# Kernel tuning notes

Hardware: AMD Instinct MI355X
Metric: run time of the kernel (lower is better)

## Reference

```python
import jax, jax.numpy as jnp
import numpy as np

K_LAYERS = 2   # top-k layers kept in zeta routing
K_EXPERTS = 2  # top-k experts kept in alpha routing


def _topk_sparse_softmax(logits, k):
    """Keep top-k along last axis, set rest to -inf, softmax. logits [..., N]."""
    lead = logits.shape[:-1]
    n = logits.shape[-1]
    flat = logits.reshape(-1, n)
    vals, idx = jax.lax.top_k(flat, k)                      # [R,k]
    sparse = jnp.full_like(flat, -jnp.inf)
    rows = jnp.arange(flat.shape[0])[:, None]
    sparse = sparse.at[rows, idx].set(vals)
    return jax.nn.softmax(sparse, axis=-1).reshape(*lead, n)


def _lora_layer(h, W, b, A, B, zeta_l, alpha_l):
    """One backbone Linear + gated LoRA expert mixture + ReLU.
    h [B,in], W [out,in], A [E,r,in], B [E,out,r], zeta_l [B], alpha_l [B,E].
    """
    lin = h @ W.T + b                                       # [B,out]
    t = jnp.einsum('bi,eri->ber', h, A)                     # [B,E,r]
    tw = t * alpha_l[:, :, None]                            # weight experts early
    lora_sum = jnp.einsum('ber,eor->bo', tw, B)             # [B,out]
    return jax.nn.relu(lin + zeta_l[:, None] * lora_sum)


def _routing(domain_ids, dom_emb, layer_pos, Wi1, bi1, Wi2, bi2,
             Wa1, ba1, Wa2, ba2, gate_logits, R_benefit):
    M, H = dom_emb.shape
    L = layer_pos.shape[0]
    router_inp = jnp.concatenate([
        jnp.broadcast_to(dom_emb[:, None, :], (M, L, H)),
        jnp.broadcast_to(layer_pos[None, :, :], (M, L, H)),
    ], axis=-1)                                             # [M,L,2H]
    hz = jax.nn.relu(router_inp @ Wi1.T + bi1)
    zeta_logits = (hz @ Wi2.T + bi2)[..., 0]                # [M,L]
    zeta_all = _topk_sparse_softmax(zeta_logits, K_LAYERS)
    ha = jax.nn.relu(router_inp @ Wa1.T + ba1)
    alpha_logits = ha @ Wa2.T + ba2                         # [M,L,E]
    alpha_all = _topk_sparse_softmax(alpha_logits, K_EXPERTS)
    # gated benefit matrix, row-normalized
    R = jax.nn.softplus(gate_logits) * R_benefit
    R = R / jnp.clip(R.sum(-1, keepdims=True), 1e-12)
    zeta_agg = R @ zeta_all                                 # [M,L]
    alpha_agg = jnp.einsum('mn,nle->mle', R, alpha_all)     # [M,L,E]
    return zeta_agg[domain_ids], alpha_agg[domain_ids]      # [B,L],[B,L,E]


def setup_inputs() -> dict:
    key = jax.random.key(0)
    ks = jax.random.split(key, 32)
    Bsz, D0, D1, D2, D3 = 16384, 2048, 2048, 1024, 512
    E, r, M, H, L = 4, 8, 8, 64, 3
    s = 0.02
    return {
        'x': jax.random.normal(ks[0], (Bsz, D0), jnp.float32),
        'domain_ids': jax.random.randint(ks[1], (Bsz,), 0, M),
        'W1': jax.random.normal(ks[2], (D1, D0)) * s, 'b1': jnp.zeros((D1,)),
        'W2': jax.random.normal(ks[3], (D2, D1)) * s, 'b2': jnp.zeros((D2,)),
        'W3': jax.random.normal(ks[4], (D3, D2)) * s, 'b3': jnp.zeros((D3,)),
        'A1': jax.random.normal(ks[5], (E, r, D0)) * s, 'B1': jax.random.normal(ks[6], (E, D1, r)) * s,
        'A2': jax.random.normal(ks[7], (E, r, D1)) * s, 'B2': jax.random.normal(ks[8], (E, D2, r)) * s,
        'A3': jax.random.normal(ks[9], (E, r, D2)) * s, 'B3': jax.random.normal(ks[10], (E, D3, r)) * s,
        'dom_emb': jax.random.normal(ks[11], (M, H)) * s,
        'layer_pos': jax.random.normal(ks[12], (L, H)) * s,
        'Wi1': jax.random.normal(ks[13], (H, 2 * H)) * 0.1, 'bi1': jnp.zeros((H,)),
        'Wi2': jax.random.normal(ks[14], (1, H)) * 0.1, 'bi2': jnp.zeros((1,)),
        'Wa1': jax.random.normal(ks[15], (H, 2 * H)) * 0.1, 'ba1': jnp.zeros((H,)),
        'Wa2': jax.random.normal(ks[16], (E, H)) * 0.1, 'ba2': jnp.zeros((E,)),
        'gate_logits': jax.random.normal(ks[17], (M, M)) * 0.1,
        'R_benefit': jax.random.uniform(ks[18], (M, M)),
    }


def reference(x, domain_ids, W1, b1, W2, b2, W3, b3,
              A1, B1, A2, B2, A3, B3,
              dom_emb, layer_pos, Wi1, bi1, Wi2, bi2,
              Wa1, ba1, Wa2, ba2, gate_logits, R_benefit):
    zeta, alpha = _routing(domain_ids, dom_emb, layer_pos, Wi1, bi1, Wi2, bi2,
                           Wa1, ba1, Wa2, ba2, gate_logits, R_benefit)
    h = _lora_layer(x, W1, b1, A1, B1, zeta[:, 0], alpha[:, 0])
    h = _lora_layer(h, W2, b2, A2, B2, zeta[:, 1], alpha[:, 1])
    h = _lora_layer(h, W3, b3, A3, B3, zeta[:, 2], alpha[:, 2])
    return h
```

## Files before the change

### kernel.cpp

```cpp
#include <hip/hip_runtime.h>

typedef __bf16 bf16_t;
typedef __bf16 bf16x8 __attribute__((ext_vector_type(8)));
typedef __bf16 bf16x4_v __attribute__((ext_vector_type(4)));
typedef float f32x4 __attribute__((ext_vector_type(4)));

#define AS1 __attribute__((address_space(1)))
#define AS3 __attribute__((address_space(3)))

__device__ __forceinline__ void gload_lds16(const void* g, void* l) {
    __builtin_amdgcn_global_load_lds((AS1 void*)(void*)g, (AS3 void*)l, 16, 0, 0);
}

__global__ void __launch_bounds__(256) prep_kernel(
    const float* __restrict__ dom_emb, const float* __restrict__ layer_pos,
    const float* __restrict__ Wi1, const float* __restrict__ bi1,
    const float* __restrict__ Wi2, const float* __restrict__ bi2,
    const float* __restrict__ Wa1, const float* __restrict__ ba1,
    const float* __restrict__ Wa2, const float* __restrict__ ba2,
    const float* __restrict__ gate_logits, const float* __restrict__ R_benefit,
    float* __restrict__ salpha,
    const float* __restrict__ s0, const float* __restrict__ s1,
    const float* __restrict__ s2, const float* __restrict__ s3,
    const float* __restrict__ s4, const float* __restrict__ s5,
    bf16_t* __restrict__ wdst,
    const float* __restrict__ B1, const float* __restrict__ B2,
    const float* __restrict__ B3, bf16_t* __restrict__ bedst)
{
    const int blk = blockIdx.x;
    const int t = threadIdx.x;
    if (blk == 0) {
        constexpr int M = 8, L = 3, E = 4, H = 64;
        __shared__ float zl[M * L];
        __shared__ float al[M * L][E];
        __shared__ float zeta_all[M][L];
        __shared__ float alpha_all[M][L][E];
        const int ml = t >> 3, js = t & 7;
        if (ml < M * L) {
            const int m = ml / L, l = ml % L;
            float zacc = 0.f;
            float aacc[E] = {0.f, 0.f, 0.f, 0.f};
            for (int jj = 0; jj < 8; ++jj) {
                const int j = js * 8 + jj;
                float hz = bi1[j], ha = ba1[j];
                for (int i = 0; i < H; ++i) {
                    const float de = dom_emb[m * H + i];
                    const float lp = layer_pos[l * H + i];
                    hz += de * Wi1[j * 2 * H + i] + lp * Wi1[j * 2 * H + H + i];
                    ha += de * Wa1[j * 2 * H + i] + lp * Wa1[j * 2 * H + H + i];
                }
                hz = fmaxf(hz, 0.f); ha = fmaxf(ha, 0.f);
                zacc += hz * Wi2[j];
                for (int e = 0; e < E; ++e) aacc[e] += ha * Wa2[e * H + j];
            }
            #pragma unroll
            for (int off = 4; off >= 1; off >>= 1) {
                zacc += __shfl_down(zacc, off, 8);
                for (int e = 0; e < E; ++e) aacc[e] += __shfl_down(aacc[e], off, 8);
            }
            if (js == 0) {
                zl[ml] = zacc + bi2[0];
                for (int e = 0; e < E; ++e) al[ml][e] = aacc[e] + ba2[e];
            }
        }
        __syncthreads();
        if (t < M) {
            const int m = t;
            float v[3] = { zl[m * L + 0], zl[m * L + 1], zl[m * L + 2] };
            int di = 0; float dv = v[0];
            for (int i = 1; i < 3; ++i) if (v[i] <= dv) { dv = v[i]; di = i; }
            float mx = -1e30f;
            for (int i = 0; i < 3; ++i) if (i != di) mx = fmaxf(mx, v[i]);
            float s = 0.f, ev[3];
            for (int i = 0; i < 3; ++i) { ev[i] = (i == di) ? 0.f : expf(v[i] - mx); s += ev[i]; }
            for (int i = 0; i < 3; ++i) zeta_all[m][i] = ev[i] / s;
            for (int l = 0; l < L; ++l) {
                float a[4];
                for (int e = 0; e < 4; ++e) a[e] = al[m * L + l][e];
                int i1 = 0;
                for (int e = 1; e < 4; ++e) if (a[e] > a[i1]) i1 = e;
                int i2 = -1;
                for (int e = 0; e < 4; ++e) { if (e == i1) continue; if (i2 < 0 || a[e] > a[i2]) i2 = e; }
                const float mx2 = fmaxf(a[i1], a[i2]);
                const float e1 = expf(a[i1] - mx2), e2 = expf(a[i2] - mx2);
                const float ss = e1 + e2;
                for (int e = 0; e < 4; ++e) alpha_all[m][l][e] = 0.f;
                alpha_all[m][l][i1] = e1 / ss;
                alpha_all[m][l][i2] = e2 / ss;
            }
        }
        __syncthreads();
        if (t < M) {
            const int m = t;
            float Rrow[8]; float rs = 0.f;
            for (int n = 0; n < M; ++n) {
                const float g = gate_logits[m * M + n];
                const float rr = log1pf(expf(g)) * R_benefit[m * M + n];
                Rrow[n] = rr; rs += rr;
            }
            rs = fmaxf(rs, 1e-12f);
            for (int l = 0; l < L; ++l) {
                float zag = 0.f, aag[4] = {0.f, 0.f, 0.f, 0.f};
                for (int n = 0; n < M; ++n) {
                    const float w = Rrow[n] / rs;
                    zag += w * zeta_all[n][l];
                    for (int e = 0; e < 4; ++e) aag[e] += w * alpha_all[n][l][e];
                }
                for (int e = 0; e < 4; ++e) salpha[(m * L + l) * 4 + e] = zag * aag[e];
            }
        }
    } else if (blk <= 6816) {
        const int i = (blk - 1) * 256 + t;
        constexpr int b0 = 1048576;
        constexpr int b1 = b0 + 524288;
        constexpr int b2 = b1 + 131072;
        constexpr int b3 = b2 + 16384;
        constexpr int b4 = b3 + 16384;
        const float* src; int rel;
        if (i < b0)      { src = s0; rel = i; }
        else if (i < b1) { src = s1; rel = i - b0; }
        else if (i < b2) { src = s2; rel = i - b1; }
        else if (i < b3) { src = s3; rel = i - b2; }
        else if (i < b4) { src = s4; rel = i - b3; }
        else             { src = s5; rel = i - b4; }
        const float4 v = ((const float4*)src)[rel];
        bf16x4_v o;
        o[0] = (__bf16)v.x; o[1] = (__bf16)v.y; o[2] = (__bf16)v.z; o[3] = (__bf16)v.w;
        ((bf16x4_v*)wdst)[i] = o;
    } else {
        const int idx = (blk - 6817) * 256 + t;
        constexpr int c1 = 2048 * 32, c2 = c1 + 1024 * 32;
        const float* B; int rel, Dout;
        if (idx < c1)      { B = B1; rel = idx;      Dout = 2048; }
        else if (idx < c2) { B = B2; rel = idx - c1; Dout = 1024; }
        else               { B = B3; rel = idx - c2; Dout = 512; }
        const int o = rel >> 5, c = rel & 31, e = c >> 3, r = c & 7;
        bedst[idx] = (__bf16)B[((size_t)e * Dout + o) * 8 + r];
    }
}

template<bool F32IN>
__global__ void __launch_bounds__(256) tw_kernel(
    const void* __restrict__ hin, bf16_t* __restrict__ xb_out,
    const bf16_t* __restrict__ Acat, const float* __restrict__ salpha,
    const int* __restrict__ dom, const int layer, const int K,
    bf16_t* __restrict__ TWb)
{
    const int t = threadIdx.x, wid = t >> 6, lane = t & 63;
    const int rb = blockIdx.x * 64 + wid * 16;
    const int ln15 = lane & 15, kg = (lane >> 4) * 8;
    const int row = rb + ln15;
    const int Kh = K >> 1;
    f32x4 a0l = {0.f,0.f,0.f,0.f}, a1l = {0.f,0.f,0.f,0.f};
    f32x4 a0h = {0.f,0.f,0.f,0.f}, a1h = {0.f,0.f,0.f,0.f};
    const bf16_t* pa0 = Acat + (size_t)ln15 * K + kg;
    const bf16_t* pa1 = pa0 + (size_t)16 * K;
    for (int k0 = 0; k0 < Kh; k0 += 32) {
        bf16x8 al, ah;
        if constexpr (F32IN) {
            const float* px = (const float*)hin + (size_t)row * K + k0 + kg;
            const float4 x0 = *(const float4*)px;
            const float4 x1 = *(const float4*)(px + 4);
            const float4 y0 = *(const float4*)(px + Kh);
            const float4 y1 = *(const float4*)(px + Kh + 4);
            al[0] = (__bf16)x0.x; al[1] = (__bf16)x0.y; al[2] = (__bf16)x0.z; al[3] = (__bf16)x0.w;
            al[4] = (__bf16)x1.x; al[5] = (__bf16)x1.y; al[6] = (__bf16)x1.z; al[7] = (__bf16)x1.w;
            ah[0] = (__bf16)y0.x; ah[1] = (__bf16)y0.y; ah[2] = (__bf16)y0.z; ah[3] = (__bf16)y0.w;
            ah[4] = (__bf16)y1.x; ah[5] = (__bf16)y1.y; ah[6] = (__bf16)y1.z; ah[7] = (__bf16)y1.w;
            *(bf16x8*)(xb_out + (size_t)row * K + k0 + kg) = al;
            *(bf16x8*)(xb_out + (size_t)row * K + Kh + k0 + kg) = ah;
        } else {
            al = *(const bf16x8*)((const bf16_t*)hin + (size_t)row * K + k0 + kg);
            ah = *(const bf16x8*)((const bf16_t*)hin + (size_t)row * K + Kh + k0 + kg);
        }
        const bf16x8 b0l = *(const bf16x8*)(pa0 + k0);
        const bf16x8 b1l = *(const bf16x8*)(pa1 + k0);
        const bf16x8 b0h = *(const bf16x8*)(pa0 + Kh + k0);
        const bf16x8 b1h = *(const bf16x8*)(pa1 + Kh + k0);
        a0l = __builtin_amdgcn_mfma_f32_16x16x32_bf16(al, b0l, a0l, 0, 0, 0);
        a1l = __builtin_amdgcn_mfma_f32_16x16x32_bf16(al, b1l, a1l, 0, 0, 0);
        a0h = __builtin_amdgcn_mfma_f32_16x16x32_bf16(ah, b0h, a0h, 0, 0, 0);
        a1h = __builtin_amdgcn_mfma_f32_16x16x32_bf16(ah, b1h, a1h, 0, 0, 0);
    }
    const f32x4 acc0 = a0l + a0h;
    const f32x4 acc1 = a1l + a1h;
    const int rbase = rb + (lane >> 4) * 4;
    #pragma unroll
    for (int i = 0; i < 4; ++i) {
        const int r2 = rbase + i;
        const int d = dom[r2];
        const float* sa = salpha + (d * 3 + layer) * 4;
        const float s0 = sa[ln15 >> 3];
        const float s1 = sa[2 + (ln15 >> 3)];
        TWb[(size_t)r2 * 32 + ln15]      = (__bf16)(acc0[i] * s0);
        TWb[(size_t)r2 * 32 + 16 + ln15] = (__bf16)(acc1[i] * s1);
    }
}


__device__ __forceinline__ void stage_chunk32(const bf16_t* g, char* chunk, int t) {
    const int row = t >> 2;
    const int sl = t & 3;
    const int src = sl ^ (((row >> 3) & 1) << 1);
    gload_lds16(g + (size_t)row * 32 + src * 8, chunk + t * 16);
}

template<int K>
__global__ void __launch_bounds__(512, 2) gemm_lora8(
    const bf16_t* __restrict__ Abuf, const bf16_t* __restrict__ Wbuf,
    const float* __restrict__ bias, const bf16_t* __restrict__ TWb,
    const bf16_t* __restrict__ Bepi, bf16_t* __restrict__ outp,
    const int N, const int nwg_n)
{
    __shared__ __align__(1024) char lds[131072];
    const int t = threadIdx.x;
    const int wid = t >> 6, lane = t & 63;
    const int wm = wid >> 2, wn = wid & 3, wnh = wn >> 1;
    const int cpx = gridDim.x >> 3;
    const int wg = (blockIdx.x & 7) * cpx + (blockIdx.x >> 3);
    const int row0 = (wg / nwg_n) * 256, col0 = (wg % nwg_n) * 256;

    const int r15 = lane & 15;
    const int swb = ((lane >> 4) ^ (((lane >> 3) & 1) << 1)) << 4;

    const char* aBase = lds + (wm << 14) + (r15 << 6) + swb;
    const char* bBase = lds + 65536 + (wnh << 14) + ((wn & 1) << 12) + (r15 << 6) + swb;
    char* const dBase = lds + t * 16;

    const int srow = t >> 2, ssl = t & 3;
    const int ssrc = ssl ^ (((srow >> 3) & 1) << 1);
    const bf16_t* sA = Abuf + (size_t)(row0 + srow) * K + ssrc * 8;
    const bf16_t* sB = Wbuf + (size_t)(col0 + srow) * K + ssrc * 8;
    constexpr size_t halfA = (size_t)128 * K;

    f32x4 acc[8][4] = {};
    bf16x8 aF[4], bF[4];

    #define RD_A(P, KQ, MB) do { _Pragma("unroll") for (int i_ = 0; i_ < 4; ++i_) \
        aF[i_] = *(const bf16x8*)(aBase + (P)*32768 + (KQ)*8192 + ((MB)+i_)*1024); } while (0)
    #define RD_B(P, KQ) do { _Pragma("unroll") for (int n_ = 0; n_ < 4; ++n_) \
        bF[n_] = *(const bf16x8*)(bBase + (P)*32768 + (KQ)*8192 + n_*1024); } while (0)

    auto mfma16 = [&](int mbase) {
        __builtin_amdgcn_s_setprio(1);
        #pragma unroll
        for (int mf = 0; mf < 4; ++mf)
            #pragma unroll
            for (int nf = 0; nf < 4; ++nf)
                acc[mbase + mf][nf] =
                    __builtin_amdgcn_mfma_f32_16x16x32_bf16(aF[mf], bF[nf], acc[mbase + mf][nf], 0, 0, 0);
        __builtin_amdgcn_s_setprio(0);
    };
    #define BAR() __builtin_amdgcn_s_barrier()

    constexpr int NT = K >> 6;

    gload_lds16(sA,              dBase + 0);
    gload_lds16(sA + halfA,      dBase + 16384);
    gload_lds16(sB,              dBase + 65536);
    gload_lds16(sB + halfA,      dBase + 65536 + 16384);
    gload_lds16(sA + 32,         dBase + 8192);
    gload_lds16(sA + halfA + 32, dBase + 24576);
    gload_lds16(sB + 32,         dBase + 65536 + 8192);
    gload_lds16(sB + halfA + 32, dBase + 65536 + 24576);
    asm volatile("s_waitcnt vmcnt(4)" ::: "memory");
    __builtin_amdgcn_s_barrier();

    const bf16_t* pA0 = sA + 64;
    const bf16_t* pA1 = sA + halfA + 64;
    const bf16_t* pB0 = sB + 64;
    const bf16_t* pB1 = sB + halfA + 64;

    #define TILE(P, MORE, TOFF) do {                                            \
        RD_A(P, 0, 0);                                                           \
        RD_B(P, 0);                                                              \
        if (MORE) { gload_lds16(pA0 + (TOFF), dBase + ((P)^1)*32768 + 0);        \
                    gload_lds16(pA1 + (TOFF), dBase + ((P)^1)*32768 + 16384); }  \
        BAR();                                                                   \
        mfma16(0);                                                               \
        RD_A(P, 0, 4);                                                           \
        if (MORE) {                                                              \
            gload_lds16(pB0 + (TOFF), dBase + 65536 + ((P)^1)*32768 + 0);        \
            gload_lds16(pB1 + (TOFF), dBase + 65536 + ((P)^1)*32768 + 16384);    \
            asm volatile("s_waitcnt vmcnt(4)" ::: "memory");                     \
        } else {                                                                 \
            asm volatile("s_waitcnt vmcnt(0)" ::: "memory");                     \
        }                                                                        \
        BAR();                                                                   \
        mfma16(4);                                                               \
        RD_A(P, 1, 4);                                                           \
        RD_B(P, 1);                                                              \
        if (MORE) { gload_lds16(pA0 + (TOFF) + 32, dBase + ((P)^1)*32768 + 8192);  \
                    gload_lds16(pA1 + (TOFF) + 32, dBase + ((P)^1)*32768 + 24576);} \
        BAR();                                                                   \
        mfma16(4);                                                               \
        RD_A(P, 1, 0);                                                           \
        if (MORE) {                                                              \
            gload_lds16(pB0 + (TOFF) + 32, dBase + 65536 + ((P)^1)*32768 + 8192);  \
            gload_lds16(pB1 + (TOFF) + 32, dBase + 65536 + ((P)^1)*32768 + 24576); \
            asm volatile("s_waitcnt vmcnt(4)" ::: "memory");                     \
        }                                                                        \
        BAR();                                                                   \
        mfma16(0);                                                               \
    } while (0)

    #pragma unroll 1
    for (int T = 0; T < NT - 2; T += 2) {
        TILE(0, true, 0);
        TILE(1, true, 64);
        pA0 += 128; pA1 += 128; pB0 += 128; pB1 += 128;
    }
    TILE(0, true, 0);
    TILE(1, false, 64);

    {
        __builtin_amdgcn_s_barrier();
        stage_chunk32(TWb + (size_t)row0 * 32,          lds + 0,             t);
        stage_chunk32(TWb + (size_t)(row0 + 128) * 32,  lds + 16384,         t);
        stage_chunk32(Bepi + (size_t)col0 * 32,         lds + 65536,         t);
        stage_chunk32(Bepi + (size_t)(col0 + 128) * 32, lds + 65536 + 16384, t);
        asm volatile("s_waitcnt vmcnt(0)" ::: "memory");
        __builtin_amdgcn_s_barrier();
        RD_B(0, 0);
        RD_A(0, 0, 0);
        mfma16(0);
        RD_A(0, 0, 4);
        mfma16(4);
    }

    __builtin_amdgcn_s_barrier();
    {
        char* eb = lds + wid * 2048;
        const int rloc = (lane >> 4) * 4;
        const int g = lane >> 4;
        const int orow0 = row0 + wm * 128;
        const int ocol0 = col0 + wn * 64;
        float bcol[4];
        #pragma unroll
        for (int nf = 0; nf < 4; ++nf) bcol[nf] = bias[ocol0 + nf * 16 + r15];
        const int rdrow = lane >> 3;
        const int rdcolb = (lane & 7) * 16;
        const int rdoff0 = rdrow * 128 + (rdcolb ^ ((rdrow >> 2) << 5));
        const int rdoff1 = (rdrow + 8) * 128 + (rdcolb ^ (((rdrow + 8) >> 2) << 5));
        bf16_t* outbase = outp + (size_t)ocol0 + (lane & 7) * 8;
        #pragma unroll
        for (int mf = 0; mf < 8; ++mf) {
            #pragma unroll
            for (int i = 0; i < 4; ++i) {
                const int r = rloc + i;
                #pragma unroll
                for (int nf = 0; nf < 4; ++nf) {
                    const float v = fmaxf(acc[mf][nf][i] + bcol[nf], 0.f);
                    *(bf16_t*)(eb + r * 128 + ((nf ^ g) * 32 + r15 * 2)) = (__bf16)v;
                }
            }
            __builtin_amdgcn_sched_barrier(0);
            asm volatile("" ::: "memory");
            const bf16x8 v0 = *(const bf16x8*)(eb + rdoff0);
            const bf16x8 v1 = *(const bf16x8*)(eb + rdoff1);
            asm volatile("" ::: "memory");
            __builtin_amdgcn_sched_barrier(0);
            *(bf16x8*)(outbase + (size_t)(orow0 + mf * 16 + rdrow) * N) = v0;
            *(bf16x8*)(outbase + (size_t)(orow0 + mf * 16 + 8 + rdrow) * N) = v1;
        }
    }
    #undef TILE
    #undef RD_A
    #undef RD_B
    #undef BAR
}

#define BM 128
#define BN 128
#define BK 32

template<bool OUT_F32, int K>
__global__ void __launch_bounds__(256) gemm_lora(
    const bf16_t* __restrict__ Abuf, const bf16_t* __restrict__ Wbuf,
    const float* __restrict__ bias, const bf16_t* __restrict__ TWb,
    const bf16_t* __restrict__ Bepi, void* __restrict__ outp,
    const int N)
{
    __shared__ bf16_t lA[BM * BK];
    __shared__ bf16_t lB[BN * BK];
    const int t = threadIdx.x;
    const int row0 = blockIdx.y * BM;
    const int col0 = blockIdx.x * BN;
    const int wid = t >> 6, lane = t & 63;
    const int wr = wid >> 1, wc = wid & 1;
    const int ln15 = lane & 15, kg = (lane >> 4) * 8;
    const int srow = t >> 2, sg8 = (t & 3) * 8;
    const bf16_t* gA = Abuf + (size_t)(row0 + srow) * K + sg8;
    const bf16_t* gB = Wbuf + (size_t)(col0 + srow) * K + sg8;
    bf16_t* ldA  = &lA[t * 8];
    bf16_t* ldA2 = &lA[2048 + t * 8];
    bf16_t* ldB  = &lB[t * 8];
    bf16_t* ldB2 = &lB[2048 + t * 8];
    f32x4 acc[4][4] = {};
    const int aoff = (wr * 64 + ln15) * BK + kg;
    const int boff = (wc * 64 + ln15) * BK + kg;

    auto compute_tile = [&]() {
        bf16x8 af[4], bfr[4];
        #pragma unroll
        for (int m = 0; m < 4; ++m) af[m] = *(const bf16x8*)&lA[aoff + m * 16 * BK];
        #pragma unroll
        for (int n = 0; n < 4; ++n) bfr[n] = *(const bf16x8*)&lB[boff + n * 16 * BK];
        #pragma unroll
        for (int m = 0; m < 4; ++m)
            #pragma unroll
            for (int n = 0; n < 4; ++n)
                acc[m][n] = __builtin_amdgcn_mfma_f32_16x16x32_bf16(af[m], bfr[n], acc[m][n], 0, 0, 0);
    };

    constexpr size_t half = (size_t)64 * K;
    constexpr int nk = K / BK;
    #pragma unroll 1
    for (int kt = 0; kt < nk; ++kt) {
        gload_lds16(gA + kt * BK, ldA);
        gload_lds16(gA + half + kt * BK, ldA2);
        gload_lds16(gB + kt * BK, ldB);
        gload_lds16(gB + half + kt * BK, ldB2);
        __syncthreads();
        compute_tile();
        __syncthreads();
    }
    gload_lds16(TWb + (size_t)(row0 + srow) * 32 + sg8, ldA);
    gload_lds16(TWb + (size_t)(row0 + 64 + srow) * 32 + sg8, ldA2);
    gload_lds16(Bepi + (size_t)(col0 + srow) * 32 + sg8, ldB);
    gload_lds16(Bepi + (size_t)(col0 + 64 + srow) * 32 + sg8, ldB2);
    __syncthreads();
    compute_tile();

    const int orow = row0 + wr * 64 + (lane >> 4) * 4;
    const int ocol = col0 + wc * 64 + ln15;
    #pragma unroll
    for (int n = 0; n < 4; ++n) {
        const int col = ocol + n * 16;
        const float bn = bias[col];
        #pragma unroll
        for (int m = 0; m < 4; ++m) {
            const int rbase = orow + m * 16;
            #pragma unroll
            for (int i = 0; i < 4; ++i) {
                const float v = fmaxf(acc[m][n][i] + bn, 0.f);
                if constexpr (OUT_F32)
                    ((float*)outp)[(size_t)(rbase + i) * N + col] = v;
                else
                    ((bf16_t*)outp)[(size_t)(rbase + i) * N + col] = (__bf16)v;
            }
        }
    }
}

extern "C" void kernel_launch(void* const* d_in, const int* in_sizes, int n_in,
                              void* d_out, int out_size, void* d_ws, size_t ws_size,
                              hipStream_t stream)
{
    const float* x    = (const float*)d_in[0];
    const int*   dom  = (const int*)d_in[1];
    const float* W1   = (const float*)d_in[2];  const float* b1  = (const float*)d_in[3];
    const float* W2   = (const float*)d_in[4];  const float* b2  = (const float*)d_in[5];
    const float* W3   = (const float*)d_in[6];  const float* b3  = (const float*)d_in[7];
    const float* A1   = (const float*)d_in[8];  const float* B1  = (const float*)d_in[9];
    const float* A2   = (const float*)d_in[10]; const float* B2  = (const float*)d_in[11];
    const float* A3   = (const float*)d_in[12]; const float* B3  = (const float*)d_in[13];
    const float* dome = (const float*)d_in[14]; const float* lpos = (const float*)d_in[15];
    const float* Wi1  = (const float*)d_in[16]; const float* bi1 = (const float*)d_in[17];
    const float* Wi2  = (const float*)d_in[18]; const float* bi2 = (const float*)d_in[19];
    const float* Wa1  = (const float*)d_in[20]; const float* ba1 = (const float*)d_in[21];
    const float* Wa2  = (const float*)d_in[22]; const float* ba2 = (const float*)d_in[23];
    const float* gate = (const float*)d_in[24]; const float* Rb  = (const float*)d_in[25];
    (void)in_sizes; (void)n_in; (void)out_size; (void)ws_size;

    constexpr int Bsz = 16384, D0 = 2048, D1 = 2048, D2 = 1024, D3 = 512;

    char* ws = (char*)d_ws;
    size_t off = 0;
    auto alloc = [&](size_t bytes) -> void* {
        void* p = ws + off;
        off = (off + bytes + 255) & ~(size_t)255;
        return p;
    };
    float*  salpha = (float*) alloc(8 * 3 * 4 * sizeof(float));
    bf16_t* W1b = (bf16_t*)alloc((size_t)D1 * D0 * 2);
    bf16_t* W2b = (bf16_t*)alloc((size_t)D2 * D1 * 2);
    bf16_t* W3b = (bf16_t*)alloc((size_t)D3 * D2 * 2);
    bf16_t* Ac1 = (bf16_t*)alloc((size_t)32 * D0 * 2);
    bf16_t* Ac2 = (bf16_t*)alloc((size_t)32 * D1 * 2);
    bf16_t* Ac3 = (bf16_t*)alloc((size_t)32 * D2 * 2);
    bf16_t* Be1 = (bf16_t*)alloc((size_t)D1 * 32 * 2);
    bf16_t* Be2 = (bf16_t*)alloc((size_t)D2 * 32 * 2);
    bf16_t* Be3 = (bf16_t*)alloc((size_t)D3 * 32 * 2);
    bf16_t* TWb = (bf16_t*)alloc((size_t)Bsz * 32 * 2);
    bf16_t* xb  = (bf16_t*)alloc((size_t)Bsz * D0 * 2);
    bf16_t* h1b = (bf16_t*)alloc((size_t)Bsz * D1 * 2);
    bf16_t* h2b = xb;

    prep_kernel<<<7265, 256, 0, stream>>>(
        dome, lpos, Wi1, bi1, Wi2, bi2, Wa1, ba1, Wa2, ba2, gate, Rb, salpha,
        W1, W2, W3, A1, A2, A3, W1b,
        B1, B2, B3, Be1);

    tw_kernel<true><<<Bsz / 64, 256, 0, stream>>>(x, xb, Ac1, salpha, dom, 0, D0, TWb);
    gemm_lora8<2048><<<(Bsz / 256) * (D1 / 256), 512, 0, stream>>>(xb, W1b, b1, TWb, Be1, h1b, D1, D1 / 256);
    tw_kernel<false><<<Bsz / 64, 256, 0, stream>>>(h1b, nullptr, Ac2, salpha, dom, 1, D1, TWb);
    gemm_lora8<2048><<<(Bsz / 256) * (D2 / 256), 512, 0, stream>>>(h1b, W2b, b2, TWb, Be2, h2b, D2, D2 / 256);
    tw_kernel<false><<<Bsz / 64, 256, 0, stream>>>(h2b, nullptr, Ac3, salpha, dom, 2, D2, TWb);
    gemm_lora<true, 1024><<<dim3(D3 / BN, Bsz / BM), 256, 0, stream>>>(h2b, W3b, b3, TWb, Be3, d_out, D3);
}
```

Before: 370.0 us.

## Move x bf16 conversion into prep kernel and split tw_kernel K across two wave groups

The fp32-to-bf16 conversion of x moves out of the first tw_kernel and into extra blocks of the prep kernel, so it runs in parallel with the weight conversions. tw_kernel now uses 512 threads, with two wave groups each covering half of K. Their partial accumulators are combined through shared memory before scaling and storing TW. This halves the serial K loop per wave and raises parallelism in the small LoRA-down kernels, at the cost of a shared-memory reduction and a barrier.

```diff
diff --git a/kernel.cpp b/kernel.cpp
--- a/kernel.cpp
+++ b/kernel.cpp
@@ -25,7 +25,8 @@
     const float* __restrict__ s4, const float* __restrict__ s5,
     bf16_t* __restrict__ wdst,
     const float* __restrict__ B1, const float* __restrict__ B2,
-    const float* __restrict__ B3, bf16_t* __restrict__ bedst)
+    const float* __restrict__ B3, bf16_t* __restrict__ bedst,
+    const float* __restrict__ x, bf16_t* __restrict__ xb)
 {
     const int blk = blockIdx.x;
     const int t = threadIdx.x;
@@ -127,7 +128,7 @@
         bf16x4_v o;
         o[0] = (__bf16)v.x; o[1] = (__bf16)v.y; o[2] = (__bf16)v.z; o[3] = (__bf16)v.w;
         ((bf16x4_v*)wdst)[i] = o;
-    } else {
+    } else if (blk <= 7264) {
         const int idx = (blk - 6817) * 256 + t;
         constexpr int c1 = 2048 * 32, c2 = c1 + 1024 * 32;
         const float* B; int rel, Dout;
@@ -136,64 +137,70 @@
         else               { B = B3; rel = idx - c2; Dout = 512; }
         const int o = rel >> 5, c = rel & 31, e = c >> 3, r = c & 7;
         bedst[idx] = (__bf16)B[((size_t)e * Dout + o) * 8 + r];
-    }
-}
-
-template<bool F32IN>
-__global__ void __launch_bounds__(256) tw_kernel(
-    const void* __restrict__ hin, bf16_t* __restrict__ xb_out,
+    } else {
+        const size_t i8 = ((size_t)(blk - 7265) * 256 + t) * 8;
+        const float4 v0 = *(const float4*)(x + i8);
+        const float4 v1 = *(const float4*)(x + i8 + 4);
+        bf16x8 o;
+        o[0] = (__bf16)v0.x; o[1] = (__bf16)v0.y; o[2] = (__bf16)v0.z; o[3] = (__bf16)v0.w;
+        o[4] = (__bf16)v1.x; o[5] = (__bf16)v1.y; o[6] = (__bf16)v1.z; o[7] = (__bf16)v1.w;
+        *(bf16x8*)(xb + i8) = o;
+    }
+}
+
+__global__ void __launch_bounds__(512) tw_kernel(
+    const bf16_t* __restrict__ hin,
     const bf16_t* __restrict__ Acat, const float* __restrict__ salpha,
     const int* __restrict__ dom, const int layer, const int K,
     bf16_t* __restrict__ TWb)
 {
+    __shared__ float red[4 * 64 * 8];
     const int t = threadIdx.x, wid = t >> 6, lane = t & 63;
-    const int rb = blockIdx.x * 64 + wid * 16;
+    const int g = wid & 3, h = wid >> 2;
+    const int rb = blockIdx.x * 64 + g * 16;
     const int ln15 = lane & 15, kg = (lane >> 4) * 8;
     const int row = rb + ln15;
-    const int Kh = K >> 1;
+    const int Kh = K >> 1, Kq = K >> 2;
+    const int base = h * Kh;
     f32x4 a0l = {0.f,0.f,0.f,0.f}, a1l = {0.f,0.f,0.f,0.f};
     f32x4 a0h = {0.f,0.f,0.f,0.f}, a1h = {0.f,0.f,0.f,0.f};
-    const bf16_t* pa0 = Acat + (size_t)ln15 * K + kg;
+    const bf16_t* ph  = hin + (size_t)row * K + base + kg;
+    const bf16_t* pa0 = Acat + (size_t)ln15 * K + base + kg;
     const bf16_t* pa1 = pa0 + (size_t)16 * K;
-    for (int k0 = 0; k0 < Kh; k0 += 32) {
-        bf16x8 al, ah;
-        if constexpr (F32IN) {
-            const float* px = (const float*)hin + (size_t)row * K + k0 + kg;
-            const float4 x0 = *(const float4*)px;
-            const float4 x1 = *(const float4*)(px + 4);
-            const float4 y0 = *(const float4*)(px + Kh);
-            const float4 y1 = *(const float4*)(px + Kh + 4);
-            al[0] = (__bf16)x0.x; al[1] = (__bf16)x0.y; al[2] = (__bf16)x0.z; al[3] = (__bf16)x0.w;
-            al[4] = (__bf16)x1.x; al[5] = (__bf16)x1.y; al[6] = (__bf16)x1.z; al[7] = (__bf16)x1.w;
-            ah[0] = (__bf16)y0.x; ah[1] = (__bf16)y0.y; ah[2] = (__bf16)y0.z; ah[3] = (__bf16)y0.w;
-            ah[4] = (__bf16)y1.x; ah[5] = (__bf16)y1.y; ah[6] = (__bf16)y1.z; ah[7] = (__bf16)y1.w;
-            *(bf16x8*)(xb_out + (size_t)row * K + k0 + kg) = al;
-            *(bf16x8*)(xb_out + (size_t)row * K + Kh + k0 + kg) = ah;
-        } else {
-            al = *(const bf16x8*)((const bf16_t*)hin + (size_t)row * K + k0 + kg);
-            ah = *(const bf16x8*)((const bf16_t*)hin + (size_t)row * K + Kh + k0 + kg);
-        }
+    for (int k0 = 0; k0 < Kq; k0 += 32) {
+        const bf16x8 al  = *(const bf16x8*)(ph + k0);
+        const bf16x8 ah  = *(const bf16x8*)(ph + Kq + k0);
         const bf16x8 b0l = *(const bf16x8*)(pa0 + k0);
         const bf16x8 b1l = *(const bf16x8*)(pa1 + k0);
-        const bf16x8 b0h = *(const bf16x8*)(pa0 + Kh + k0);
-        const bf16x8 b1h = *(const bf16x8*)(pa1 + Kh + k0);
+        const bf16x8 b0h = *(const bf16x8*)(pa0 + Kq + k0);
+        const bf16x8 b1h = *(const bf16x8*)(pa1 + Kq + k0);
         a0l = __builtin_amdgcn_mfma_f32_16x16x32_bf16(al, b0l, a0l, 0, 0, 0);
         a1l = __builtin_amdgcn_mfma_f32_16x16x32_bf16(al, b1l, a1l, 0, 0, 0);
         a0h = __builtin_amdgcn_mfma_f32_16x16x32_bf16(ah, b0h, a0h, 0, 0, 0);
         a1h = __builtin_amdgcn_mfma_f32_16x16x32_bf16(ah, b1h, a1h, 0, 0, 0);
     }
-    const f32x4 acc0 = a0l + a0h;
-    const f32x4 acc1 = a1l + a1h;
-    const int rbase = rb + (lane >> 4) * 4;
-    #pragma unroll
-    for (int i = 0; i < 4; ++i) {
-        const int r2 = rbase + i;
-        const int d = dom[r2];
-        const float* sa = salpha + (d * 3 + layer) * 4;
-        const float s0 = sa[ln15 >> 3];
-        const float s1 = sa[2 + (ln15 >> 3)];
-        TWb[(size_t)r2 * 32 + ln15]      = (__bf16)(acc0[i] * s0);
-        TWb[(size_t)r2 * 32 + 16 + ln15] = (__bf16)(acc1[i] * s1);
+    f32x4 acc0 = a0l + a0h;
+    f32x4 acc1 = a1l + a1h;
+    float* slot = red + ((g * 64 + lane) << 3);
+    if (h == 1) {
+        *(f32x4*)slot = acc0;
+        *(f32x4*)(slot + 4) = acc1;
+    }
+    __syncthreads();
+    if (h == 0) {
+        acc0 += *(const f32x4*)slot;
+        acc1 += *(const f32x4*)(slot + 4);
+        const int rbase = rb + (lane >> 4) * 4;
+        #pragma unroll
+        for (int i = 0; i < 4; ++i) {
+            const int r2 = rbase + i;
+            const int d = dom[r2];
+            const float* sa = salpha + (d * 3 + layer) * 4;
+            const float s0 = sa[ln15 >> 3];
+            const float s1 = sa[2 + (ln15 >> 3)];
+            TWb[(size_t)r2 * 32 + ln15]      = (__bf16)(acc0[i] * s0);
+            TWb[(size_t)r2 * 32 + 16 + ln15] = (__bf16)(acc1[i] * s1);
+        }
     }
 }
 
@@ -497,15 +504,16 @@
     bf16_t* h1b = (bf16_t*)alloc((size_t)Bsz * D1 * 2);
     bf16_t* h2b = xb;
 
-    prep_kernel<<<7265, 256, 0, stream>>>(
+    prep_kernel<<<23649, 256, 0, stream>>>(
         dome, lpos, Wi1, bi1, Wi2, bi2, Wa1, ba1, Wa2, ba2, gate, Rb, salpha,
         W1, W2, W3, A1, A2, A3, W1b,
-        B1, B2, B3, Be1);
-
-    tw_kernel<true><<<Bsz / 64, 256, 0, stream>>>(x, xb, Ac1, salpha, dom, 0, D0, TWb);
+        B1, B2, B3, Be1,
+        x, xb);
+
+    tw_kernel<<<Bsz / 64, 512, 0, stream>>>(xb, Ac1, salpha, dom, 0, D0, TWb);
     gemm_lora8<2048><<<(Bsz / 256) * (D1 / 256), 512, 0, stream>>>(xb, W1b, b1, TWb, Be1, h1b, D1, D1 / 256);
-    tw_kernel<false><<<Bsz / 64, 256, 0, stream>>>(h1b, nullptr, Ac2, salpha, dom, 1, D1, TWb);
+    tw_kernel<<<Bsz / 64, 512, 0, stream>>>(h1b, Ac2, salpha, dom, 1, D1, TWb);
     gemm_lora8<2048><<<(Bsz / 256) * (D2 / 256), 512, 0, stream>>>(h1b, W2b, b2, TWb, Be2, h2b, D2, D2 / 256);
-    tw_kernel<false><<<Bsz / 64, 256, 0, stream>>>(h2b, nullptr, Ac3, salpha, dom, 2, D2, TWb);
+    tw_kernel<<<Bsz / 64, 512, 0, stream>>>(h2b, Ac3, salpha, dom, 2, D2, TWb);
     gemm_lora<true, 1024><<<dim3(D3 / BN, Bsz / BM), 256, 0, stream>>>(h2b, W3b, b3, TWb, Be3, d_out, D3);
 }
```

Result: faster. 358.8 us (-3.0%).
